# Kernel tuning notes

Hardware: AMD Instinct MI355X
Metric: run time of the kernel (lower is better)

## Reference

```python
import jax, jax.numpy as jnp
import numpy as np

N_HEADS, N_LEVELS, N_POINTS = 8, 3, 4


def _bilinear_sample(valf, Hl, Wl, grid):
    """torch.F.grid_sample(mode='bilinear', padding_mode='zeros', align_corners=False).
    valf: [B, nH, hd, Hl*Wl] flattened per-head value map
    grid: [B, Q, nH, P, 2] normalized (x, y) in [-1, 1]
    returns [B, nH, hd, Q, P]
    """
    B, Q, nH, P, _ = grid.shape
    hd = valf.shape[2]
    # unnormalize (align_corners=False)
    ix = ((grid[..., 0] + 1.0) * Wl - 1.0) * 0.5  # [B,Q,nH,P]
    iy = ((grid[..., 1] + 1.0) * Hl - 1.0) * 0.5
    x0 = jnp.floor(ix); y0 = jnp.floor(iy)
    x1 = x0 + 1.0;      y1 = y0 + 1.0
    # corner weights
    w00 = (x1 - ix) * (y1 - iy)
    w01 = (ix - x0) * (y1 - iy)
    w10 = (x1 - ix) * (iy - y0)
    w11 = (ix - x0) * (iy - y0)

    def gather(xi, yi):
        inb = (xi >= 0) & (xi <= Wl - 1) & (yi >= 0) & (yi <= Hl - 1)  # zero padding
        xc = jnp.clip(xi, 0, Wl - 1).astype(jnp.int32)
        yc = jnp.clip(yi, 0, Hl - 1).astype(jnp.int32)
        idx = yc * Wl + xc                              # [B,Q,nH,P]
        idx = idx.transpose(0, 2, 1, 3).reshape(B, nH, 1, Q * P)
        idx = jnp.broadcast_to(idx, (B, nH, hd, Q * P))
        g = jnp.take_along_axis(valf, idx, axis=3)      # [B,nH,hd,Q*P]
        g = g.reshape(B, nH, hd, Q, P)
        mask = inb.transpose(0, 2, 1, 3)[:, :, None, :, :]
        return g * mask

    def w_(w):  # [B,Q,nH,P] -> [B,nH,1,Q,P]
        return w.transpose(0, 2, 1, 3)[:, :, None, :, :]

    return (gather(x0, y0) * w_(w00) + gather(x1, y0) * w_(w01)
            + gather(x0, y1) * w_(w10) + gather(x1, y1) * w_(w11))


def _deform_attn(query, feats, reference_points,
                 W_off, b_off, W_attn, b_attn, W_val, b_val, W_out, b_out):
    B, Q, D = query.shape
    nH, L, P = N_HEADS, N_LEVELS, N_POINTS
    hd = D // nH
    # sampling offsets: tanh * 0.5
    off = jnp.tanh(query @ W_off + b_off).reshape(B, Q, nH, L, P, 2) * 0.5
    # attention weights: softmax over levels*points
    aw = jax.nn.softmax((query @ W_attn + b_attn).reshape(B, Q, nH, L * P), axis=-1)
    aw = aw.reshape(B, Q, nH, L, P)

    out = jnp.zeros((B, Q, nH, hd), dtype=query.dtype)
    for lvl, feat in enumerate(feats):
        Hl, Wl = feat.shape[2], feat.shape[3]
        # value projection on flattened map
        v = feat.reshape(B, D, Hl * Wl).transpose(0, 2, 1) @ W_val + b_val  # [B,S,D]
        valf = v.reshape(B, Hl * Wl, nH, hd).transpose(0, 2, 3, 1)          # [B,nH,hd,S]
        grid = (reference_points[:, :, None, None, :] + off[:, :, :, lvl]) * 2.0 - 1.0  # [B,Q,nH,P,2]
        sampled = _bilinear_sample(valf, Hl, Wl, grid)                      # [B,nH,hd,Q,P]
        w = aw[:, :, :, lvl].transpose(0, 2, 1, 3)[:, :, None, :, :]        # [B,nH,1,Q,P]
        out = out + (sampled * w).sum(-1).transpose(0, 3, 1, 2)             # [B,Q,nH,hd]
    return out.reshape(B, Q, D) @ W_out + b_out


def setup_inputs() -> dict:
    key = jax.random.key(0)
    ks = jax.random.split(key, 13)
    B, Q, D = 4, 8400, 256
    return {
        "query": jax.random.normal(ks[0], (B, Q, D), jnp.float32),
        "feat0": jax.random.normal(ks[1], (B, D, 80, 80), jnp.float32),
        "feat1": jax.random.normal(ks[2], (B, D, 40, 40), jnp.float32),
        "feat2": jax.random.normal(ks[3], (B, D, 20, 20), jnp.float32),
        "reference_points": jax.random.uniform(ks[4], (B, Q, 2), jnp.float32),
        "W_off": jax.random.normal(ks[5], (D, N_HEADS * N_LEVELS * N_POINTS * 2), jnp.float32) * 0.02,
        "b_off": jax.random.normal(ks[6], (N_HEADS * N_LEVELS * N_POINTS * 2,), jnp.float32) * 0.02,
        "W_attn": jax.random.normal(ks[7], (D, N_HEADS * N_LEVELS * N_POINTS), jnp.float32) * 0.02,
        "b_attn": jax.random.normal(ks[8], (N_HEADS * N_LEVELS * N_POINTS,), jnp.float32) * 0.02,
        "W_val": jax.random.normal(ks[9], (D, D), jnp.float32) * (1.0 / np.sqrt(D)),
        "b_val": jnp.zeros((D,), jnp.float32),
        "W_out": jax.random.normal(ks[10], (D, D), jnp.float32) * (1.0 / np.sqrt(D)),
        "b_out": jnp.zeros((D,), jnp.float32),
    }


def reference(query, feat0, feat1, feat2, reference_points,
              W_off, b_off, W_attn, b_attn, W_val, b_val, W_out, b_out):
    return _deform_attn(query, [feat0, feat1, feat2], reference_points,
                        W_off, b_off, W_attn, b_attn, W_val, b_val, W_out, b_out)
```

## Files before the change

kernel.cpp:

```cpp
#include <hip/hip_runtime.h>
#include <math.h>

#define NH    8
#define DIM   256
#define NQ    8400
#define BATCH 4
#define STOT  8400
#define MQ    (BATCH * NQ)

typedef _Float16 f16;
typedef __attribute__((ext_vector_type(2))) _Float16 f16x2;
typedef __attribute__((ext_vector_type(8))) _Float16 f16x8;
typedef __attribute__((ext_vector_type(4))) float  f32x4;

static __device__ __forceinline__ void gl_lds16(const void* g, void* l) {
    __builtin_amdgcn_global_load_lds(
        (const __attribute__((address_space(1))) unsigned int*)g,
        (__attribute__((address_space(3))) unsigned int*)(unsigned int)(unsigned long long)l,
        16, 0, 0);
}

__global__ __launch_bounds__(256) void prep_w(
    const float* __restrict__ W_val, const float* __restrict__ W_out,
    const float* __restrict__ W_off, const float* __restrict__ W_attn,
    const float* __restrict__ b_off, const float* __restrict__ b_attn,
    f16* __restrict__ Wvt, f16* __restrict__ Wot, f16* __restrict__ Wch,
    float* __restrict__ bcat)
{
    const int xb = blockIdx.x;
    const int t = threadIdx.x;
    __shared__ float tile[32][33];
    const int c = t & 31, r = t >> 5;

    if (xb == 25) {
        if (blockIdx.y == 0)
            for (int i = t; i < 288; i += 256)
                bcat[i] = (i < 192) ? b_off[i] : b_attn[i - 192];
        return;
    }
    const float* W; f16* oH; int Nw, n0, nb;
    if (xb < 8)       { W = W_val;  oH = Wvt; Nw = 256; n0 = 0;   nb = xb * 32; }
    else if (xb < 16) { W = W_out;  oH = Wot; Nw = 256; n0 = 0;   nb = (xb - 8) * 32; }
    else if (xb < 22) { W = W_off;  oH = Wch; Nw = 192; n0 = 0;   nb = (xb - 16) * 32; }
    else              { W = W_attn; oH = Wch; Nw = 96;  n0 = 192; nb = (xb - 22) * 32; }
    const int k0 = blockIdx.y * 32;
    #pragma unroll
    for (int i = 0; i < 4; ++i) {
        int k = k0 + r + i * 8, n = nb + c;
        tile[r + i * 8][c] = (n < Nw) ? W[(size_t)k * Nw + n] : 0.f;
    }
    __syncthreads();
    #pragma unroll
    for (int i = 0; i < 4; ++i) {
        int n = nb + r + i * 8, k = k0 + c;
        if (n < Nw)
            oH[(size_t)(n0 + n) * 256 + k] = (f16)tile[c][r + i * 8];
    }
}

template<int KIND>
__global__ __launch_bounds__(256) void gemm_fused(
    const float* __restrict__ feat0, const float* __restrict__ feat1,
    const float* __restrict__ feat2, const float* __restrict__ query,
    const f16* __restrict__ A16,
    const f16* __restrict__ B0, const f16* __restrict__ B1,
    const float* __restrict__ bias0, const float* __restrict__ bias1,
    f16* __restrict__ valh, float* __restrict__ rawo, f16* __restrict__ attnh,
    float* __restrict__ Cf)
{
    __shared__ __align__(16) f16 Ahs[128 * 40];
    __shared__ __align__(16) f16 Bs[128 * 32];

    const bool split = (KIND == 0) && (blockIdx.x >= 2);
    const int bn = split ? (blockIdx.x - 2) * 128 : blockIdx.x * 128;
    const int bm = blockIdx.y * 128;
    const int N = split ? 288 : 256;
    const f16* Bg = split ? B1 : B0;
    const float* bias = split ? bias1 : bias0;

    const int t = threadIdx.x;
    const int lane = t & 63, w = t >> 6;
    const int wm = (w & 1) * 64, wn = (w >> 1) * 64;
    const int l15 = lane & 15, quad = lane >> 4;

    const int fstage = ((t >> 2) & 3) ^ ((t >> 4) & 3);
    const int qs = (t & 3) ^ fstage;
    const int ffrag = (l15 & 3) ^ ((l15 >> 2) & 3);
    const int qf = quad ^ ffrag;

    const float* aptr = nullptr; int Sv = 0;
    int rA0 = 0, kqA = 0;
    if (KIND == 0 && !split) {
        const int spair = t >> 2;
        kqA = t & 3;
        rA0 = spair * 2;
        int gr = bm + rA0;
        if (gr + 1 >= MQ) gr = MQ - 2;
        int bb = gr / STOT, s = gr - bb * STOT;
        if (s < 6400)      { aptr = feat0 + (size_t)bb * 256 * 6400 + s;          Sv = 6400; }
        else if (s < 8000) { aptr = feat1 + (size_t)bb * 256 * 1600 + (s - 6400); Sv = 1600; }
        else               { aptr = feat2 + (size_t)bb * 256 * 400  + (s - 8000); Sv = 400;  }
    }

    f32x4 acc[4][4];
    #pragma unroll
    for (int i = 0; i < 4; ++i)
        #pragma unroll
        for (int j = 0; j < 4; ++j)
            acc[i][j] = (f32x4){0.f, 0.f, 0.f, 0.f};

    for (int k0 = 0; k0 < 256; k0 += 32) {
        if (KIND == 0 && !split) {
            float2 va[8];
            #pragma unroll
            for (int j = 0; j < 8; ++j)
                va[j] = *(const float2*)(aptr + (size_t)(k0 + kqA * 8 + j) * Sv);
            f16x8 h0, h1;
            #pragma unroll
            for (int j = 0; j < 8; ++j) { h0[j] = (f16)va[j].x; h1[j] = (f16)va[j].y; }
            *(f16x8*)&Ahs[((rA0)     * 5 + kqA) * 8] = h0;
            *(f16x8*)&Ahs[((rA0 + 1) * 5 + kqA) * 8] = h1;
        } else if (KIND == 0) {
            #pragma unroll
            for (int i = 0; i < 2; ++i) {
                int row = i * 64 + (t >> 2), q4 = t & 3;
                int gr = bm + row; if (gr > MQ - 1) gr = MQ - 1;
                const float* qp = query + (size_t)gr * 256 + k0 + q4 * 8;
                float4 a = *(const float4*)qp;
                float4 b = *(const float4*)(qp + 4);
                f16x8 h;
                h[0] = (f16)a.x; h[1] = (f16)a.y; h[2] = (f16)a.z; h[3] = (f16)a.w;
                h[4] = (f16)b.x; h[5] = (f16)b.y; h[6] = (f16)b.z; h[7] = (f16)b.w;
                *(f16x8*)&Ahs[(row * 5 + q4) * 8] = h;
            }
        } else {
            #pragma unroll
            for (int i = 0; i < 2; ++i) {
                int row = i * 64 + (t >> 2), slot = i * 256 + t;
                int gr = bm + row; if (gr > MQ - 1) gr = MQ - 1;
                gl_lds16(A16 + (size_t)gr * 256 + k0 + qs * 8, &Ahs[slot * 8]);
            }
        }
        #pragma unroll
        for (int i = 0; i < 2; ++i) {
            int row = i * 64 + (t >> 2), slot = i * 256 + t;
            int gn = bn + row; if (gn > N - 1) gn = N - 1;
            gl_lds16(Bg + (size_t)gn * 256 + k0 + qs * 8, &Bs[slot * 8]);
        }
        __syncthreads();

        f16x8 af[4], bfv[4];
        #pragma unroll
        for (int mt = 0; mt < 4; ++mt) {
            int ar = wm + mt * 16 + l15;
            af[mt] = (KIND == 0)
                ? *(const f16x8*)&Ahs[(ar * 5 + quad) * 8]
                : *(const f16x8*)&Ahs[(ar * 4 + qf) * 8];
        }
        #pragma unroll
        for (int nt = 0; nt < 4; ++nt)
            bfv[nt] = *(const f16x8*)&Bs[((wn + nt * 16 + l15) * 4 + qf) * 8];
        #pragma unroll
        for (int mt = 0; mt < 4; ++mt)
            #pragma unroll
            for (int nt = 0; nt < 4; ++nt)
                acc[mt][nt] = __builtin_amdgcn_mfma_f32_16x16x32_f16(af[mt], bfv[nt], acc[mt][nt], 0, 0, 0);
        __syncthreads();
    }

    #pragma unroll
    for (int nt = 0; nt < 4; ++nt) {
        int col = bn + wn + nt * 16 + l15;
        float bv = (col < N) ? bias[col] : 0.f;
        #pragma unroll
        for (int mt = 0; mt < 4; ++mt) {
            int row0 = bm + wm + mt * 16 + quad * 4;
            #pragma unroll
            for (int r = 0; r < 4; ++r) {
                int row = row0 + r;
                if (row >= MQ || col >= N) continue;
                float v = acc[mt][nt][r] + bv;
                if (KIND == 1) {
                    Cf[(size_t)row * 256 + col] = v;
                } else if (!split) {
                    int bb = row / STOT, s = row - bb * STOT;
                    int h = col >> 5, c = col & 31;
                    valh[(((size_t)(bb * 8 + h)) * STOT + s) * 32 + c] = (f16)v;
                } else if (col < 192) {
                    rawo[(size_t)row * 192 + col] = 0.5f * tanhf(v);
                } else {
                    attnh[(size_t)row * 96 + (col - 192)] = (f16)v;
                }
            }
        }
    }
}

__global__ __launch_bounds__(256) void sample_v7(
    const f16* __restrict__ valh,
    const float* __restrict__ off05,
    const f16* __restrict__ attnh,
    const float* __restrict__ refp,
    f16* __restrict__ out_h)
{
    const int bx = blockIdx.x;
    const int xcd = bx & 7;
    const int b = xcd >> 1;
    const int qi = (bx >> 3) * 2 + (xcd & 1);
    const int bq0 = b * NQ + qi * 8;
    const int t = threadIdx.x;

    __shared__ unsigned s_pk[8][96][4];
    __shared__ float    s_m[8][8];
    __shared__ float    s_inv[8][8];

    if (t < 64) {
        int q = t >> 3, h = t & 7;
        const f16* a = attnh + (size_t)(bq0 + q) * 96 + h * 12;
        float m = (float)a[0];
        #pragma unroll
        for (int j = 1; j < 12; ++j) m = fmaxf(m, (float)a[j]);
        float s = 0.f;
        #pragma unroll
        for (int j = 0; j < 12; ++j) s += expf((float)a[j] - m);
        s_m[q][h] = m;
        s_inv[q][h] = 1.f / s;
    }
    __syncthreads();

    for (int i = t; i < 768; i += 256) {
        int q = i / 96, p = i - q * 96;
        int h = p / 12, lp = p - h * 12, l = lp >> 2;
        const int dims[3]   = {80, 40, 20};
        const int bases_[3] = {0, 6400, 8000};
        int Wl = dims[l], base = bases_[l];
        float logit = (float)attnh[(size_t)(bq0 + q) * 96 + p];
        float aw = expf(logit - s_m[q][h]) * s_inv[q][h];
        size_t ro = (size_t)(bq0 + q) * 192 + h * 24 + lp * 2;
        float ox = off05[ro], oy = off05[ro + 1];
        float rx = refp[(size_t)(bq0 + q) * 2];
        float ry = refp[(size_t)(bq0 + q) * 2 + 1];
        float ix = (rx + ox) * Wl - 0.5f;
        float iy = (ry + oy) * Wl - 0.5f;
        float x0f = floorf(ix), y0f = floorf(iy);
        float fx = ix - x0f, fy = iy - y0f;
        int x0 = (int)x0f, y0 = (int)y0f;
        float w00 = (1.f - fx) * (1.f - fy) * aw;
        float w01 = fx * (1.f - fy) * aw;
        float w10 = (1.f - fx) * fy * aw;
        float w11 = fx * fy * aw;
        bool vx0 = (unsigned)x0 < (unsigned)Wl;
        bool vx1 = (unsigned)(x0 + 1) < (unsigned)Wl;
        bool vy0 = (unsigned)y0 < (unsigned)Wl;
        bool vy1 = (unsigned)(y0 + 1) < (unsigned)Wl;
        int row0 = base + y0 * Wl, row1 = row0 + Wl;
        float ws[4] = { vx0 && vy0 ? w00 : 0.f, vx1 && vy0 ? w01 : 0.f,
                        vx0 && vy1 ? w10 : 0.f, vx1 && vy1 ? w11 : 0.f };
        int   is[4] = { vx0 && vy0 ? row0 + x0 : 0, vx1 && vy0 ? row0 + x0 + 1 : 0,
                        vx0 && vy1 ? row1 + x0 : 0, vx1 && vy1 ? row1 + x0 + 1 : 0 };
        #pragma unroll
        for (int k = 0; k < 4; ++k) {
            unsigned short us = __builtin_bit_cast(unsigned short, (f16)ws[k]);
            s_pk[q][p][k] = ((unsigned)us << 16) | (unsigned)is[k];
        }
    }
    __syncthreads();

    const int q = t >> 5;
    const int h = (t >> 2) & 7;
    const int l4 = t & 3;
    const uint4* vb4 = (const uint4*)(valh + (size_t)(b * 8 + h) * STOT * 32);
    const unsigned* pkp = &s_pk[q][h * 12][0];
    float accf[8] = {};
    #pragma unroll
    for (int pp = 0; pp < 4; ++pp) {
        unsigned pk[12]; uint4 v[12];
        #pragma unroll
        for (int k = 0; k < 12; ++k) pk[k] = pkp[pp * 12 + k];
        #pragma unroll
        for (int k = 0; k < 12; ++k) v[k] = vb4[(size_t)(pk[k] & 0xffffu) * 4 + l4];
        f16x2 a0 = (f16x2)(f16)0, a1 = a0, a2 = a0, a3 = a0;
        #pragma unroll
        for (int k = 0; k < 12; ++k) {
            f16x2 wv = __builtin_bit_cast(f16x2,
                        __builtin_amdgcn_perm(pk[k], pk[k], 0x03020302u));
            a0 += wv * __builtin_bit_cast(f16x2, v[k].x);
            a1 += wv * __builtin_bit_cast(f16x2, v[k].y);
            a2 += wv * __builtin_bit_cast(f16x2, v[k].z);
            a3 += wv * __builtin_bit_cast(f16x2, v[k].w);
        }
        accf[0] += (float)a0[0]; accf[1] += (float)a0[1];
        accf[2] += (float)a1[0]; accf[3] += (float)a1[1];
        accf[4] += (float)a2[0]; accf[5] += (float)a2[1];
        accf[6] += (float)a3[0]; accf[7] += (float)a3[1];
    }
    f16x8 ob;
    #pragma unroll
    for (int c = 0; c < 8; ++c) ob[c] = (f16)accf[c];
    *(f16x8*)(out_h + (size_t)(bq0 + q) * 256 + h * 32 + l4 * 8) = ob;
}

extern "C" void kernel_launch(void* const* d_in, const int* in_sizes, int n_in,
                              void* d_out, int out_size, void* d_ws, size_t ws_size,
                              hipStream_t stream)
{
    const float* query  = (const float*)d_in[0];
    const float* feat0  = (const float*)d_in[1];
    const float* feat1  = (const float*)d_in[2];
    const float* feat2  = (const float*)d_in[3];
    const float* refp   = (const float*)d_in[4];
    const float* W_off  = (const float*)d_in[5];
    const float* b_off  = (const float*)d_in[6];
    const float* W_attn = (const float*)d_in[7];
    const float* b_attn = (const float*)d_in[8];
    const float* W_val  = (const float*)d_in[9];
    const float* b_val  = (const float*)d_in[10];
    const float* W_out  = (const float*)d_in[11];
    const float* b_out  = (const float*)d_in[12];
    float* out = (float*)d_out;

    f16*   valh  = (f16*)d_ws;
    float* rawo  = (float*)(valh + (size_t)MQ * 256);
    f16*   attnh = (f16*)(rawo + (size_t)MQ * 192);
    f16*   outh  = attnh + (size_t)MQ * 96;
    f16*   Wvt   = outh + (size_t)MQ * 256;
    f16*   Wot   = Wvt + 65536;
    f16*   Wch   = Wot + 65536;
    float* bcat  = (float*)(Wch + 73728);

    dim3 blk(256);

    prep_w<<<dim3(26, 8), blk, 0, stream>>>(W_val, W_out, W_off, W_attn,
                                            b_off, b_attn, Wvt, Wot, Wch, bcat);
    gemm_fused<0><<<dim3(5, 263), blk, 0, stream>>>(feat0, feat1, feat2, query, nullptr,
                                                    Wvt, Wch, b_val, bcat,
                                                    valh, rawo, attnh, nullptr);
    sample_v7<<<dim3(MQ / 8), blk, 0, stream>>>(valh, rawo, attnh, refp, outh);
    gemm_fused<1><<<dim3(2, 263), blk, 0, stream>>>(feat0, feat1, feat2, query, outh,
                                                    Wot, nullptr, b_out, nullptr,
                                                    nullptr, nullptr, nullptr, out);
}
```

Measured before the change: 257.2 us.

## Double-buffer LDS tiles in fused GEMM to overlap global loads with MFMA

Shared-memory A and B tiles are duplicated into two buffers. The next K-slice is loaded (into registers for the fp32-converted paths, directly into LDS for the async paths) while MFMAs consume the current buffer, and one barrier per iteration is removed. The intent is to hide global-load latency behind compute. In exchange, LDS use doubles, register pressure rises from the prefetched values, and occupancy may drop.

```diff
diff --git a/kernel.cpp b/kernel.cpp
--- a/kernel.cpp
+++ b/kernel.cpp
@@ -68,8 +68,8 @@
     f16* __restrict__ valh, float* __restrict__ rawo, f16* __restrict__ attnh,
     float* __restrict__ Cf)
 {
-    __shared__ __align__(16) f16 Ahs[128 * 40];
-    __shared__ __align__(16) f16 Bs[128 * 32];
+    __shared__ __align__(16) f16 Ahs[2][128 * 40];
+    __shared__ __align__(16) f16 Bs[2][128 * 32];
 
     const bool split = (KIND == 0) && (blockIdx.x >= 2);
     const int bn = split ? (blockIdx.x - 2) * 128 : blockIdx.x * 128;
@@ -89,11 +89,10 @@
     const int qf = quad ^ ffrag;
 
     const float* aptr = nullptr; int Sv = 0;
-    int rA0 = 0, kqA = 0;
+    int rA0 = 0;
+    const int kqA = t & 3;
     if (KIND == 0 && !split) {
-        const int spair = t >> 2;
-        kqA = t & 3;
-        rA0 = spair * 2;
+        rA0 = (t >> 2) * 2;
         int gr = bm + rA0;
         if (gr + 1 >= MQ) gr = MQ - 2;
         int bb = gr / STOT, s = gr - bb * STOT;
@@ -102,70 +101,102 @@
         else               { aptr = feat2 + (size_t)bb * 256 * 400  + (s - 8000); Sv = 400;  }
     }
 
-    f32x4 acc[4][4];
-    #pragma unroll
-    for (int i = 0; i < 4; ++i)
-        #pragma unroll
-        for (int j = 0; j < 4; ++j)
-            acc[i][j] = (f32x4){0.f, 0.f, 0.f, 0.f};
-
-    for (int k0 = 0; k0 < 256; k0 += 32) {
-        if (KIND == 0 && !split) {
-            float2 va[8];
-            #pragma unroll
-            for (int j = 0; j < 8; ++j)
-                va[j] = *(const float2*)(aptr + (size_t)(k0 + kqA * 8 + j) * Sv);
-            f16x8 h0, h1;
-            #pragma unroll
-            for (int j = 0; j < 8; ++j) { h0[j] = (f16)va[j].x; h1[j] = (f16)va[j].y; }
-            *(f16x8*)&Ahs[((rA0)     * 5 + kqA) * 8] = h0;
-            *(f16x8*)&Ahs[((rA0 + 1) * 5 + kqA) * 8] = h1;
-        } else if (KIND == 0) {
-            #pragma unroll
-            for (int i = 0; i < 2; ++i) {
-                int row = i * 64 + (t >> 2), q4 = t & 3;
-                int gr = bm + row; if (gr > MQ - 1) gr = MQ - 1;
-                const float* qp = query + (size_t)gr * 256 + k0 + q4 * 8;
-                float4 a = *(const float4*)qp;
-                float4 b = *(const float4*)(qp + 4);
-                f16x8 h;
-                h[0] = (f16)a.x; h[1] = (f16)a.y; h[2] = (f16)a.z; h[3] = (f16)a.w;
-                h[4] = (f16)b.x; h[5] = (f16)b.y; h[6] = (f16)b.z; h[7] = (f16)b.w;
-                *(f16x8*)&Ahs[(row * 5 + q4) * 8] = h;
-            }
-        } else {
-            #pragma unroll
-            for (int i = 0; i < 2; ++i) {
-                int row = i * 64 + (t >> 2), slot = i * 256 + t;
-                int gr = bm + row; if (gr > MQ - 1) gr = MQ - 1;
-                gl_lds16(A16 + (size_t)gr * 256 + k0 + qs * 8, &Ahs[slot * 8]);
-            }
-        }
+    float2 va[8];
+    float4 qa[4];
+
+    auto loadA_val = [&](int k0) {
+        #pragma unroll
+        for (int j = 0; j < 8; ++j)
+            va[j] = *(const float2*)(aptr + (size_t)(k0 + kqA * 8 + j) * Sv);
+    };
+    auto writeA_val = [&](int buf) {
+        f16x8 h0, h1;
+        #pragma unroll
+        for (int j = 0; j < 8; ++j) { h0[j] = (f16)va[j].x; h1[j] = (f16)va[j].y; }
+        *(f16x8*)&Ahs[buf][((rA0)     * 5 + kqA) * 8] = h0;
+        *(f16x8*)&Ahs[buf][((rA0 + 1) * 5 + kqA) * 8] = h1;
+    };
+    auto loadA_q = [&](int k0) {
+        #pragma unroll
+        for (int i = 0; i < 2; ++i) {
+            int row = i * 64 + (t >> 2);
+            int gr = bm + row; if (gr > MQ - 1) gr = MQ - 1;
+            const float* qp = query + (size_t)gr * 256 + k0 + kqA * 8;
+            qa[i * 2]     = *(const float4*)qp;
+            qa[i * 2 + 1] = *(const float4*)(qp + 4);
+        }
+    };
+    auto writeA_q = [&](int buf) {
+        #pragma unroll
+        for (int i = 0; i < 2; ++i) {
+            int row = i * 64 + (t >> 2);
+            float4 a = qa[i * 2], b = qa[i * 2 + 1];
+            f16x8 h;
+            h[0] = (f16)a.x; h[1] = (f16)a.y; h[2] = (f16)a.z; h[3] = (f16)a.w;
+            h[4] = (f16)b.x; h[5] = (f16)b.y; h[6] = (f16)b.z; h[7] = (f16)b.w;
+            *(f16x8*)&Ahs[buf][(row * 5 + kqA) * 8] = h;
+        }
+    };
+    auto stageA_lds = [&](int k0, int buf) {
+        #pragma unroll
+        for (int i = 0; i < 2; ++i) {
+            int row = i * 64 + (t >> 2), slot = i * 256 + t;
+            int gr = bm + row; if (gr > MQ - 1) gr = MQ - 1;
+            gl_lds16(A16 + (size_t)gr * 256 + k0 + qs * 8, &Ahs[buf][slot * 8]);
+        }
+    };
+    auto stageB = [&](int k0, int buf) {
         #pragma unroll
         for (int i = 0; i < 2; ++i) {
             int row = i * 64 + (t >> 2), slot = i * 256 + t;
             int gn = bn + row; if (gn > N - 1) gn = N - 1;
-            gl_lds16(Bg + (size_t)gn * 256 + k0 + qs * 8, &Bs[slot * 8]);
-        }
-        __syncthreads();
-
+            gl_lds16(Bg + (size_t)gn * 256 + k0 + qs * 8, &Bs[buf][slot * 8]);
+        }
+    };
+
+    f32x4 acc[4][4];
+    #pragma unroll
+    for (int i = 0; i < 4; ++i)
+        #pragma unroll
+        for (int j = 0; j < 4; ++j)
+            acc[i][j] = (f32x4){0.f, 0.f, 0.f, 0.f};
+
+    if (KIND == 0 && !split)      { loadA_val(0); stageB(0, 0); writeA_val(0); }
+    else if (KIND == 0)           { loadA_q(0);   stageB(0, 0); writeA_q(0); }
+    else                          { stageA_lds(0, 0); stageB(0, 0); }
+    __syncthreads();
+
+    #pragma unroll
+    for (int kt = 0; kt < 8; ++kt) {
+        const int cur = kt & 1, nxt = cur ^ 1;
+        const int k0n = (kt + 1) * 32;
+        if (kt < 7) {
+            if (KIND == 0 && !split)  loadA_val(k0n);
+            else if (KIND == 0)       loadA_q(k0n);
+            else                      stageA_lds(k0n, nxt);
+            stageB(k0n, nxt);
+        }
         f16x8 af[4], bfv[4];
         #pragma unroll
         for (int mt = 0; mt < 4; ++mt) {
             int ar = wm + mt * 16 + l15;
             af[mt] = (KIND == 0)
-                ? *(const f16x8*)&Ahs[(ar * 5 + quad) * 8]
-                : *(const f16x8*)&Ahs[(ar * 4 + qf) * 8];
+                ? *(const f16x8*)&Ahs[cur][(ar * 5 + quad) * 8]
+                : *(const f16x8*)&Ahs[cur][(ar * 4 + qf) * 8];
         }
         #pragma unroll
         for (int nt = 0; nt < 4; ++nt)
-            bfv[nt] = *(const f16x8*)&Bs[((wn + nt * 16 + l15) * 4 + qf) * 8];
+            bfv[nt] = *(const f16x8*)&Bs[cur][((wn + nt * 16 + l15) * 4 + qf) * 8];
         #pragma unroll
         for (int mt = 0; mt < 4; ++mt)
             #pragma unroll
             for (int nt = 0; nt < 4; ++nt)
                 acc[mt][nt] = __builtin_amdgcn_mfma_f32_16x16x32_f16(af[mt], bfv[nt], acc[mt][nt], 0, 0, 0);
-        __syncthreads();
+        if (kt < 7) {
+            if (KIND == 0 && !split)  writeA_val(nxt);
+            else if (KIND == 0)       writeA_q(nxt);
+            __syncthreads();
+        }
     }
 
     #pragma unroll
```

Result: faster. 248.4 us (-3.4%).
